# Kernel optimization log

Hardware: AMD Instinct MI355X
Metric: run time of the kernel (lower is better)

Reference implementation:

```python
import jax, jax.numpy as jnp
import numpy as np

N_NODES = 50000
N_EDGES = 800000
NUM_GRAPHS = 250
NODES_PER_GRAPH = 200  # max_len for to_dense_batch
IN_DIM = 128
H1 = 128
H2 = 128
LSTM_H = 128
OUT_DIM = 2
NEG_SLOPE = 0.2  # PyG GATConv default leaky relu slope


def setup_inputs() -> dict:
    key = jax.random.key(0)
    ks = jax.random.split(key, 16)
    x = jax.random.normal(ks[0], (N_NODES, IN_DIM), dtype=jnp.float32)
    edge_index = jax.random.randint(ks[1], (2, N_EDGES), 0, N_NODES, dtype=jnp.int32)
    batch = (jnp.arange(N_NODES, dtype=jnp.int32) // NODES_PER_GRAPH)
    g = lambda k, shp, fan: jax.random.normal(k, shp, dtype=jnp.float32) / np.sqrt(fan)
    return {
        "x": x,
        "edge_index": edge_index,
        "batch": batch,
        "W_gat": g(ks[2], (IN_DIM, H1), IN_DIM),
        "a_src": g(ks[3], (H1,), H1),
        "a_dst": g(ks[4], (H1,), H1),
        "b_gat": jnp.zeros((H1,), jnp.float32),
        "W_gcn": g(ks[5], (H1, H2), H1),
        "b_gcn": jnp.zeros((H2,), jnp.float32),
        "W_ih": g(ks[6], (4 * LSTM_H, H2), H2),
        "W_hh": g(ks[7], (4 * LSTM_H, LSTM_H), LSTM_H),
        "b_ih": jnp.zeros((4 * LSTM_H,), jnp.float32),
        "b_hh": jnp.zeros((4 * LSTM_H,), jnp.float32),
        "W_fc": g(ks[8], (LSTM_H, OUT_DIM), LSTM_H),
        "b_fc": jnp.zeros((OUT_DIM,), jnp.float32),
    }


def _add_self_loops(edge_index, n):
    loop = jnp.arange(n, dtype=edge_index.dtype)
    src = jnp.concatenate([edge_index[0], loop])
    dst = jnp.concatenate([edge_index[1], loop])
    return src, dst


def _gat_conv(x, edge_index, W, a_src, a_dst, b):
    n = x.shape[0]
    h = x @ W                                  # [N, H1]
    src, dst = _add_self_loops(edge_index, n)
    alpha_s = h @ a_src                        # [N]
    alpha_d = h @ a_dst
    e = alpha_s[src] + alpha_d[dst]            # [E+N]
    e = jnp.where(e > 0, e, NEG_SLOPE * e)     # leaky relu
    # softmax over edges sharing the same destination node
    m = jax.ops.segment_max(e, dst, num_segments=n)
    ex = jnp.exp(e - m[dst])
    denom = jax.ops.segment_sum(ex, dst, num_segments=n)
    alpha = ex / denom[dst]
    out = jax.ops.segment_sum(h[src] * alpha[:, None], dst, num_segments=n)
    return out + b


def _gcn_conv(x, edge_index, W, b):
    n = x.shape[0]
    h = x @ W                                  # [N, H2]
    src, dst = _add_self_loops(edge_index, n)
    deg = jax.ops.segment_sum(jnp.ones_like(dst, dtype=h.dtype), dst, num_segments=n)
    dinv = jax.lax.rsqrt(jnp.maximum(deg, 1.0))
    coef = dinv[src] * dinv[dst]               # symmetric normalization
    out = jax.ops.segment_sum(h[src] * coef[:, None], dst, num_segments=n)
    return out + b


def _to_dense_batch(x, batch, num_graphs, max_len):
    n = x.shape[0]
    ones = jnp.ones((n,), jnp.int32)
    counts = jax.ops.segment_sum(ones, batch, num_segments=num_graphs)
    starts = jnp.cumsum(counts) - counts
    pos = jnp.arange(n, dtype=jnp.int32) - starts[batch]
    padded = jnp.zeros((num_graphs, max_len, x.shape[1]), x.dtype)
    padded = padded.at[batch, pos].set(x)
    return padded, counts


def _lstm_last_hidden(padded, lengths, W_ih, W_hh, b_ih, b_hh):
    B, T, D = padded.shape
    H = W_hh.shape[1]
    xs = jnp.swapaxes(padded, 0, 1)            # [T, B, D]

    def step(carry, x_t):
        h, c = carry
        gates = x_t @ W_ih.T + b_ih + h @ W_hh.T + b_hh
        i, f, g, o = jnp.split(gates, 4, axis=-1)
        c = jax.nn.sigmoid(f) * c + jax.nn.sigmoid(i) * jnp.tanh(g)
        h = jax.nn.sigmoid(o) * jnp.tanh(c)
        return (h, c), h

    init = (jnp.zeros((B, H), padded.dtype), jnp.zeros((B, H), padded.dtype))
    _, hs = jax.lax.scan(step, init, xs)       # hs: [T, B, H]
    # packed-sequence semantics: hidden state at each graph's last valid step
    return hs[lengths - 1, jnp.arange(B)]


def reference(x, edge_index, batch, W_gat, a_src, a_dst, b_gat, W_gcn, b_gcn,
              W_ih, W_hh, b_ih, b_hh, W_fc, b_fc):
    h = jax.nn.relu(_gat_conv(x, edge_index, W_gat, a_src, a_dst, b_gat))
    h = jax.nn.relu(_gcn_conv(h, edge_index, W_gcn, b_gcn))
    padded, lengths = _to_dense_batch(h, batch, NUM_GRAPHS, NODES_PER_GRAPH)
    g_rep = _lstm_last_hidden(padded, lengths, W_ih, W_hh, b_ih, b_hh)
    return g_rep @ W_fc + b_fc
```

## Files before the change

### kernel.cpp

```cpp
#include <hip/hip_runtime.h>
#include <cstddef>

#define NN 50000
#define NE 800000
#define NG 250
#define TT 200
#define DD 128
#define GH 512
#define NEG_SLOPE 0.2f
#define NCHUNK 4
#define CLEN 50
#define CAP 128
#define PSTRIDE 136
#define CSTRIDE 132
#define GRIDM ((NG * TT + 63) / 64)

typedef __attribute__((ext_vector_type(8))) short bf16x8;
typedef __attribute__((ext_vector_type(4))) float f32x4;

static __device__ __forceinline__ float fsig(float x) { return 1.0f / (1.0f + __expf(-x)); }
static __device__ __forceinline__ float ftanh(float x) {
    float e = __expf(2.0f * x);
    return 1.0f - 2.0f / (e + 1.0f);
}
static __device__ __forceinline__ unsigned short f2bf(float f) {
    unsigned int u = __float_as_uint(f);
    return (unsigned short)((u + 0x7fffu + ((u >> 16) & 1u)) >> 16);
}
static __device__ __forceinline__ float bf2f(unsigned short b) {
    return __uint_as_float(((unsigned int)b) << 16);
}

static __device__ __forceinline__ void gll16(const void* src, void* ldsdst) {
    __builtin_amdgcn_global_load_lds(
        (const __attribute__((address_space(1))) void*)src,
        (__attribute__((address_space(3))) void*)ldsdst, 16, 0, 0);
}

__global__ void k_init(int* cnt, int* gstart, int n, int ng1) {
    int i = blockIdx.x * 256 + threadIdx.x;
    if (i < n) cnt[i] = 1;
    if (i < ng1) gstart[i] = n;
}

__global__ __launch_bounds__(256) void k_prep(
    const float* __restrict__ Wgat, float* __restrict__ WgatT,
    const float* __restrict__ Wgcn, float* __restrict__ WgcnT,
    const float* __restrict__ Wih, unsigned short* __restrict__ wih_hi,
    unsigned short* __restrict__ wih_lo)
{
    int i = blockIdx.x * 256 + threadIdx.x;
    if (i < 16384) {
        int b = i >> 7, k = i & 127;
        WgatT[b * DD + k] = Wgat[k * DD + b];
    } else if (i < 32768) {
        int j = i - 16384, b = j >> 7, k = j & 127;
        WgcnT[b * DD + k] = Wgcn[k * DD + b];
    }
    float v = Wih[i];
    unsigned short hi = f2bf(v);
    wih_hi[i] = hi;
    wih_lo[i] = f2bf(v - bf2f(hi));
}

__global__ __launch_bounds__(256) void k_gemm(
    const float* __restrict__ A, const float* __restrict__ B, float* __restrict__ C,
    int M, int N, int t0, int clen, int rowsPerGraph,
    const float* __restrict__ bias1, const float* __restrict__ bias2,
    unsigned short* __restrict__ Cbf,
    float* __restrict__ as_out, float* __restrict__ ad_out,
    const float* __restrict__ a_src, const float* __restrict__ a_dst)
{
    __shared__ float4 As[2][1024];
    __shared__ float4 Bs[2][1024];
    const int tid = threadIdx.x;
    const int wv = tid >> 6;
    const int m0 = blockIdx.x * 128, n0 = blockIdx.y * 128;
    const int tr = tid >> 4, tc = tid & 15;

    float acc[8][8];
    #pragma unroll
    for (int i = 0; i < 8; ++i)
        #pragma unroll
        for (int j = 0; j < 8; ++j) acc[i][j] = 0.f;

    auto stageA = [&](int buf, int k0) {
        #pragma unroll
        for (int it = 0; it < 4; ++it) {
            int f4 = it * 256 + tid;
            int r = f4 >> 3;
            int c4s = (f4 & 7) ^ (r & 7);
            int gr = m0 + r;
            float* dst = (float*)&As[buf][it * 256 + wv * 64];
            if (gr < M) {
                int flat = (gr / clen) * rowsPerGraph + t0 + (gr % clen);
                gll16(A + (size_t)flat * DD + k0 + c4s * 4, dst);
            }
        }
    };
    auto stageB = [&](int buf, int k0) {
        #pragma unroll
        for (int it = 0; it < 4; ++it) {
            int f4 = it * 256 + tid;
            int r = f4 >> 3;
            int c4s = (f4 & 7) ^ (r & 7);
            int gn = n0 + r;
            float* dst = (float*)&Bs[buf][it * 256 + wv * 64];
            if (gn < N) gll16(B + (size_t)gn * DD + k0 + c4s * 4, dst);
        }
    };

    stageA(0, 0); stageB(0, 0);
    __syncthreads();
    int buf = 0;
    const int axor = tr & 7;
    const int bxor = tc & 7;
    for (int ks = 0; ks < 4; ++ks) {
        if (ks < 3) { stageA(buf ^ 1, (ks + 1) * 32); stageB(buf ^ 1, (ks + 1) * 32); }
        const float4* Af = &As[buf][0];
        const float4* Bf = &Bs[buf][0];
        #pragma unroll 1
        for (int k4 = 0; k4 < 8; ++k4) {
            float4 a[8], b[8];
            #pragma unroll
            for (int i = 0; i < 8; ++i) a[i] = Af[(tr + i * 16) * 8 + (k4 ^ axor)];
            #pragma unroll
            for (int j = 0; j < 8; ++j) b[j] = Bf[(tc + j * 16) * 8 + (k4 ^ bxor)];
            #pragma unroll
            for (int i = 0; i < 8; ++i)
                #pragma unroll
                for (int j = 0; j < 8; ++j)
                    acc[i][j] += a[i].x * b[j].x + a[i].y * b[j].y + a[i].z * b[j].z + a[i].w * b[j].w;
        }
        __syncthreads();
        buf ^= 1;
    }

    if (as_out) {
        float asv[8], adv[8];
        #pragma unroll
        for (int j = 0; j < 8; ++j) { asv[j] = a_src[tc + 16 * j]; adv[j] = a_dst[tc + 16 * j]; }
        #pragma unroll
        for (int i = 0; i < 8; ++i) {
            float s = 0.f, d = 0.f;
            #pragma unroll
            for (int j = 0; j < 8; ++j) { s += acc[i][j] * asv[j]; d += acc[i][j] * adv[j]; }
            #pragma unroll
            for (int off = 1; off < 16; off <<= 1) { s += __shfl_xor(s, off); d += __shfl_xor(d, off); }
            int gr = m0 + tr + i * 16;
            if (tc == 0 && gr < M) { as_out[gr] = s; ad_out[gr] = d; }
        }
    }

    #pragma unroll
    for (int i = 0; i < 8; ++i) {
        int gr = m0 + tr + i * 16;
        if (gr >= M) continue;
        #pragma unroll
        for (int j = 0; j < 8; ++j) {
            int gn = n0 + tc + j * 16;
            if (gn >= N) continue;
            float v = acc[i][j];
            if (bias1) v += bias1[gn];
            if (bias2) v += bias2[gn];
            if (Cbf) Cbf[(size_t)gr * N + gn] = f2bf(v);
            else     C[(size_t)gr * N + gn] = v;
        }
    }
}

__global__ __launch_bounds__(256) void k_gemm_mx(
    const unsigned short* __restrict__ Ahi, const unsigned short* __restrict__ Alo,
    const unsigned short* __restrict__ Bhi, const unsigned short* __restrict__ Blo,
    float* __restrict__ C, int M,
    const float* __restrict__ bias1, const float* __restrict__ bias2)
{
    __shared__ unsigned short AsH[64 * 128];
    __shared__ unsigned short AsL[64 * 128];
    __shared__ float Cs[64 * CSTRIDE];
    const int tid = threadIdx.x;
    const int wv = tid >> 6;
    const int l = tid & 63;
    const int m0 = blockIdx.x * 64;
    const int wr = (wv >> 1) * 32, wc = (wv & 1) * 64;
    const int lr = l & 15, kg = l >> 4;

    #pragma unroll
    for (int it = 0; it < 4; ++it) {
        int f = it * 256 + tid;
        int r = f >> 4, c8 = f & 15;
        int c8s = c8 ^ (r & 15);
        int gr = m0 + r;
        unsigned short* dstH = &AsH[(it * 256 + wv * 64) * 8];
        unsigned short* dstL = &AsL[(it * 256 + wv * 64) * 8];
        if (gr < M) {
            gll16(Ahi + (size_t)gr * DD + c8s * 8, dstH);
            gll16(Alo + (size_t)gr * DD + c8s * 8, dstL);
        }
    }
    __syncthreads();

    #pragma unroll 1
    for (int cg = 0; cg < 4; ++cg) {
        const int n0 = cg * 128;
        f32x4 acc[2][4];
        #pragma unroll
        for (int rt = 0; rt < 2; ++rt)
            #pragma unroll
            for (int ct = 0; ct < 4; ++ct) acc[rt][ct] = (f32x4){0.f, 0.f, 0.f, 0.f};

        #pragma unroll 1
        for (int ks = 0; ks < 4; ++ks) {
            const int qc = ks * 4 + kg;
            bf16x8 bhi[4], blo[4];
            #pragma unroll
            for (int ct = 0; ct < 4; ++ct) {
                size_t boff = (size_t)(n0 + wc + ct * 16 + lr) * DD + qc * 8;
                bhi[ct] = *(const bf16x8*)(Bhi + boff);
                blo[ct] = *(const bf16x8*)(Blo + boff);
            }
            bf16x8 ahi[2], alo[2];
            #pragma unroll
            for (int rt = 0; rt < 2; ++rt) {
                int row = wr + rt * 16 + lr;
                int slot = row * 16 + (qc ^ (row & 15));
                ahi[rt] = *(const bf16x8*)(&AsH[slot * 8]);
                alo[rt] = *(const bf16x8*)(&AsL[slot * 8]);
            }
            #pragma unroll
            for (int rt = 0; rt < 2; ++rt)
                #pragma unroll
                for (int ct = 0; ct < 4; ++ct) {
                    acc[rt][ct] = __builtin_amdgcn_mfma_f32_16x16x32_bf16(ahi[rt], bhi[ct], acc[rt][ct], 0, 0, 0);
                    acc[rt][ct] = __builtin_amdgcn_mfma_f32_16x16x32_bf16(alo[rt], bhi[ct], acc[rt][ct], 0, 0, 0);
                    acc[rt][ct] = __builtin_amdgcn_mfma_f32_16x16x32_bf16(ahi[rt], blo[ct], acc[rt][ct], 0, 0, 0);
                }
        }

        __syncthreads();
        #pragma unroll
        for (int ct = 0; ct < 4; ++ct) {
            int col = wc + ct * 16 + lr;
            float bsum = bias1[n0 + col] + bias2[n0 + col];
            #pragma unroll
            for (int rt = 0; rt < 2; ++rt) {
                int row = wr + rt * 16 + kg * 4;
                #pragma unroll
                for (int r = 0; r < 4; ++r)
                    Cs[(row + r) * CSTRIDE + col] = acc[rt][ct][r] + bsum;
            }
        }
        __syncthreads();
        #pragma unroll
        for (int it = 0; it < 8; ++it) {
            int f4 = it * 256 + tid;
            int r = f4 >> 5, c4 = f4 & 31;
            int gr = m0 + r;
            if (gr < M)
                *(float4*)(C + (size_t)gr * GH + n0 + c4 * 4) = *(const float4*)(&Cs[r * CSTRIDE + c4 * 4]);
        }
    }
}

__global__ __launch_bounds__(256) void k_gemm_mx128(
    const float* __restrict__ A, const float* __restrict__ Bw,
    unsigned short* __restrict__ Cbf, int M,
    float* __restrict__ as_out, float* __restrict__ ad_out,
    const float* __restrict__ a_src, const float* __restrict__ a_dst)
{
    __shared__ float4 As[4096];
    const int tid = threadIdx.x;
    const int wv = tid >> 6;
    const int l = tid & 63;
    const int lr = l & 15, kg = l >> 4;
    const int m0 = blockIdx.x * 128;
    const int rowbase = wv * 32;

    #pragma unroll
    for (int it = 0; it < 16; ++it) {
        int f4 = it * 256 + tid;
        int r = f4 >> 5, c4 = f4 & 31;
        int c4s = c4 ^ (r & 7);
        int gr = m0 + r;
        float* dst = (float*)&As[it * 256 + wv * 64];
        if (gr < M) gll16(A + (size_t)gr * DD + c4s * 4, dst);
    }
    __syncthreads();

    f32x4 acc[2][8];
    #pragma unroll
    for (int rt = 0; rt < 2; ++rt)
        #pragma unroll
        for (int ct = 0; ct < 8; ++ct) acc[rt][ct] = (f32x4){0.f, 0.f, 0.f, 0.f};

    #pragma unroll 1
    for (int ks = 0; ks < 4; ++ks) {
        bf16x8 bh[8];
        #pragma unroll
        for (int ct = 0; ct < 8; ++ct) {
            const float* brow = Bw + (size_t)(ct * 16 + lr) * DD + ks * 32 + kg * 8;
            float4 f0 = *(const float4*)brow;
            float4 f1 = *(const float4*)(brow + 4);
            float ff[8] = {f0.x, f0.y, f0.z, f0.w, f1.x, f1.y, f1.z, f1.w};
            #pragma unroll
            for (int j = 0; j < 8; ++j) bh[ct][j] = (short)f2bf(ff[j]);
        }
        bf16x8 ahi[2], alo[2];
        #pragma unroll
        for (int rt = 0; rt < 2; ++rt) {
            int row = rowbase + rt * 16 + lr;
            int qb = ks * 8 + kg * 2;
            float4 f0 = As[row * 32 + (qb ^ (row & 7))];
            float4 f1 = As[row * 32 + ((qb + 1) ^ (row & 7))];
            float ff[8] = {f0.x, f0.y, f0.z, f0.w, f1.x, f1.y, f1.z, f1.w};
            #pragma unroll
            for (int j = 0; j < 8; ++j) {
                unsigned short hi = f2bf(ff[j]);
                ahi[rt][j] = (short)hi;
                alo[rt][j] = (short)f2bf(ff[j] - bf2f(hi));
            }
        }
        #pragma unroll
        for (int rt = 0; rt < 2; ++rt)
            #pragma unroll
            for (int ct = 0; ct < 8; ++ct) {
                acc[rt][ct] = __builtin_amdgcn_mfma_f32_16x16x32_bf16(ahi[rt], bh[ct], acc[rt][ct], 0, 0, 0);
                acc[rt][ct] = __builtin_amdgcn_mfma_f32_16x16x32_bf16(alo[rt], bh[ct], acc[rt][ct], 0, 0, 0);
            }
    }
    #pragma unroll 1
    for (int ks = 0; ks < 4; ++ks) {
        bf16x8 bl[8];
        #pragma unroll
        for (int ct = 0; ct < 8; ++ct) {
            const float* brow = Bw + (size_t)(ct * 16 + lr) * DD + ks * 32 + kg * 8;
            float4 f0 = *(const float4*)brow;
            float4 f1 = *(const float4*)(brow + 4);
            float ff[8] = {f0.x, f0.y, f0.z, f0.w, f1.x, f1.y, f1.z, f1.w};
            #pragma unroll
            for (int j = 0; j < 8; ++j)
                bl[ct][j] = (short)f2bf(ff[j] - bf2f(f2bf(ff[j])));
        }
        bf16x8 ahi[2];
        #pragma unroll
        for (int rt = 0; rt < 2; ++rt) {
            int row = rowbase + rt * 16 + lr;
            int qb = ks * 8 + kg * 2;
            float4 f0 = As[row * 32 + (qb ^ (row & 7))];
            float4 f1 = As[row * 32 + ((qb + 1) ^ (row & 7))];
            float ff[8] = {f0.x, f0.y, f0.z, f0.w, f1.x, f1.y, f1.z, f1.w};
            #pragma unroll
            for (int j = 0; j < 8; ++j) ahi[rt][j] = (short)f2bf(ff[j]);
        }
        #pragma unroll
        for (int rt = 0; rt < 2; ++rt)
            #pragma unroll
            for (int ct = 0; ct < 8; ++ct)
                acc[rt][ct] = __builtin_amdgcn_mfma_f32_16x16x32_bf16(ahi[rt], bl[ct], acc[rt][ct], 0, 0, 0);
    }

    #pragma unroll
    for (int rt = 0; rt < 2; ++rt)
        #pragma unroll
        for (int ct = 0; ct < 8; ++ct) {
            int row = m0 + rowbase + rt * 16 + kg * 4;
            int col = ct * 16 + lr;
            #pragma unroll
            for (int r = 0; r < 4; ++r)
                if (row + r < M) Cbf[(size_t)(row + r) * DD + col] = f2bf(acc[rt][ct][r]);
        }
    if (as_out) {
        #pragma unroll
        for (int rt = 0; rt < 2; ++rt)
            #pragma unroll
            for (int r = 0; r < 4; ++r) {
                float s = 0.f, d = 0.f;
                #pragma unroll
                for (int ct = 0; ct < 8; ++ct) {
                    int col = ct * 16 + lr;
                    s += acc[rt][ct][r] * a_src[col];
                    d += acc[rt][ct][r] * a_dst[col];
                }
                #pragma unroll
                for (int off = 1; off < 16; off <<= 1) {
                    s += __shfl_xor(s, off);
                    d += __shfl_xor(d, off);
                }
                int row = m0 + rowbase + rt * 16 + kg * 4 + r;
                if (lr == 0 && row < M) { as_out[row] = s; ad_out[row] = d; }
            }
    }
}

__global__ void k_hist(const int* __restrict__ ei, int* cnt, int E) {
    int e = blockIdx.x * 256 + threadIdx.x;
    if (e < E) atomicAdd(&cnt[ei[E + e]], 1);
}

__global__ __launch_bounds__(256) void k_scan1(const int* __restrict__ cnt, int* __restrict__ fill,
                                               int* __restrict__ bsum, int n) {
    __shared__ int wsum[4];
    int tid = threadIdx.x, lane = tid & 63, wv = tid >> 6;
    int i = blockIdx.x * 256 + tid;
    int v = (i < n) ? cnt[i] : 0;
    int sc = v;
    #pragma unroll
    for (int off = 1; off < 64; off <<= 1) {
        int t = __shfl_up(sc, off);
        if (lane >= off) sc += t;
    }
    if (lane == 63) wsum[wv] = sc;
    __syncthreads();
    int base = 0;
    if (wv > 0) base += wsum[0];
    if (wv > 1) base += wsum[1];
    if (wv > 2) base += wsum[2];
    if (i < n) fill[i] = base + sc - v;
    if (tid == 255) bsum[blockIdx.x] = base + sc;
}
__global__ __launch_bounds__(256) void k_scan2(int* __restrict__ bsum, int nb) {
    __shared__ int wsum[4];
    int tid = threadIdx.x, lane = tid & 63, wv = tid >> 6;
    int v = (tid < nb) ? bsum[tid] : 0;
    int sc = v;
    #pragma unroll
    for (int off = 1; off < 64; off <<= 1) {
        int t = __shfl_up(sc, off);
        if (lane >= off) sc += t;
    }
    if (lane == 63) wsum[wv] = sc;
    __syncthreads();
    int base = 0;
    if (wv > 0) base += wsum[0];
    if (wv > 1) base += wsum[1];
    if (wv > 2) base += wsum[2];
    if (tid < nb) bsum[tid] = base + sc - v;
}
__global__ void k_scan3(const int* __restrict__ bsum, const int* __restrict__ cnt,
                        int* __restrict__ rp, int* __restrict__ fill,
                        float* __restrict__ dinv, const int* __restrict__ batch,
                        int* __restrict__ gstart, int n) {
    int i = blockIdx.x * 256 + threadIdx.x;
    if (i >= n) return;
    int v = fill[i] + bsum[blockIdx.x];
    rp[i] = v;
    fill[i] = v;
    if (i == n - 1) rp[n] = v + cnt[i];
    dinv[i] = rsqrtf(fmaxf((float)cnt[i], 1.0f));
    int b = batch[i];
    if (i == 0 || batch[i - 1] != b) gstart[b] = i;
}

__global__ void k_fill(const int* __restrict__ ei, int* fill, int* esrc, int E, int N) {
    int i = blockIdx.x * 256 + threadIdx.x;
    if (i < E) {
        int s = ei[i], d = ei[E + i];
        int slot = atomicAdd(&fill[d], 1);
        esrc[slot] = s;
    } else if (i < E + N) {
        int v = i - E;
        int slot = atomicAdd(&fill[v], 1);
        esrc[slot] = v;
    }
}

__global__ __launch_bounds__(256) void k_gat(
    const unsigned int* __restrict__ h1b,
    const float* __restrict__ as, const float* __restrict__ ad_,
    const int* __restrict__ rp, const int* __restrict__ esrc,
    const float* __restrict__ bias, float* __restrict__ out, int n)
{
    __shared__ float2 ws_sh[4][CAP];
    int wv = threadIdx.x >> 6;
    int node = blockIdx.x * 4 + wv;
    int lane = threadIdx.x & 63;
    if (node >= n) return;
    int r0 = rp[node], r1 = rp[node + 1];
    int deg = r1 - r0;
    float adv = ad_[node];

    float sum = 0.f;
    for (int base = 0; base < deg; base += 64) {
        int idx = base + lane;
        float ex = 0.f;
        if (idx < deg) {
            int s = esrc[r0 + idx];
            float e = as[s] + adv;
            e = e > 0.f ? e : NEG_SLOPE * e;
            ex = __expf(e);
            if (idx < CAP) ws_sh[wv][idx] = make_float2(ex, __int_as_float(s));
        }
        sum += ex;
    }
    #pragma unroll
    for (int off = 1; off < 64; off <<= 1) sum += __shfl_xor(sum, off);
    float inv = 1.0f / sum;

    int nser = deg < CAP ? deg : CAP;
    int npad = (nser + 7) & ~7;
    for (int p = nser + lane; p < npad; p += 64)
        ws_sh[wv][p] = make_float2(0.f, __int_as_float(0));

    float ax = 0.f, ay = 0.f;
    float wa[8]; unsigned int va[8];
    #pragma unroll
    for (int u = 0; u < 8; ++u) {
        float2 t = ws_sh[wv][u];
        wa[u] = t.x; va[u] = h1b[(size_t)__float_as_int(t.y) * 64 + lane];
    }
    #pragma unroll 1
    for (int idx = 8; idx < npad; idx += 8) {
        float wb[8]; unsigned int vb[8];
        #pragma unroll
        for (int u = 0; u < 8; ++u) {
            float2 t = ws_sh[wv][idx + u];
            wb[u] = t.x; vb[u] = h1b[(size_t)__float_as_int(t.y) * 64 + lane];
        }
        #pragma unroll
        for (int u = 0; u < 8; ++u) {
            ax += wa[u] * __uint_as_float(va[u] << 16);
            ay += wa[u] * __uint_as_float(va[u] & 0xffff0000u);
        }
        #pragma unroll
        for (int u = 0; u < 8; ++u) { wa[u] = wb[u]; va[u] = vb[u]; }
    }
    #pragma unroll
    for (int u = 0; u < 8; ++u) {
        ax += wa[u] * __uint_as_float(va[u] << 16);
        ay += wa[u] * __uint_as_float(va[u] & 0xffff0000u);
    }

    for (int j = r0 + CAP; j < r1; ++j) {
        int s = esrc[j];
        float e = as[s] + adv;
        e = e > 0.f ? e : NEG_SLOPE * e;
        float w = __expf(e);
        unsigned int v = h1b[(size_t)s * 64 + lane];
        ax += w * __uint_as_float(v << 16);
        ay += w * __uint_as_float(v & 0xffff0000u);
    }
    float2 bv = *(const float2*)(bias + 2 * lane);
    float2 o;
    o.x = fmaxf(ax * inv + bv.x, 0.f);
    o.y = fmaxf(ay * inv + bv.y, 0.f);
    *(float2*)(out + (size_t)node * DD + 2 * lane) = o;
}

__global__ __launch_bounds__(256) void k_gcn(
    const unsigned int* __restrict__ h2b, const float* __restrict__ dinv,
    const int* __restrict__ rp, const int* __restrict__ esrc,
    const float* __restrict__ bias, const int* __restrict__ batch,
    const int* __restrict__ gstart, float* __restrict__ padded,
    unsigned short* __restrict__ ph, unsigned short* __restrict__ pl, int n)
{
    __shared__ float2 cs_sh[4][CAP];
    int wv = threadIdx.x >> 6;
    int node = blockIdx.x * 4 + wv;
    int lane = threadIdx.x & 63;
    if (node >= n) return;
    int r0 = rp[node], r1 = rp[node + 1];
    int deg = r1 - r0;
    float dn = dinv[node];

    for (int base = 0; base < deg; base += 64) {
        int idx = base + lane;
        if (idx < deg && idx < CAP) {
            int s = esrc[r0 + idx];
            cs_sh[wv][idx] = make_float2(dinv[s], __int_as_float(s));
        }
    }
    int nser = deg < CAP ? deg : CAP;
    int npad = (nser + 7) & ~7;
    for (int p = nser + lane; p < npad; p += 64)
        cs_sh[wv][p] = make_float2(0.f, __int_as_float(0));
    __syncthreads();

    float ax = 0.f, ay = 0.f;
    float wa[8]; unsigned int va[8];
    #pragma unroll
    for (int u = 0; u < 8; ++u) {
        float2 t = cs_sh[wv][u];
        wa[u] = t.x; va[u] = h2b[(size_t)__float_as_int(t.y) * 64 + lane];
    }
    #pragma unroll 1
    for (int idx = 8; idx < npad; idx += 8) {
        float wb[8]; unsigned int vb[8];
        #pragma unroll
        for (int u = 0; u < 8; ++u) {
            float2 t = cs_sh[wv][idx + u];
            wb[u] = t.x; vb[u] = h2b[(size_t)__float_as_int(t.y) * 64 + lane];
        }
        #pragma unroll
        for (int u = 0; u < 8; ++u) {
            ax += wa[u] * __uint_as_float(va[u] << 16);
            ay += wa[u] * __uint_as_float(va[u] & 0xffff0000u);
        }
        #pragma unroll
        for (int u = 0; u < 8; ++u) { wa[u] = wb[u]; va[u] = vb[u]; }
    }
    #pragma unroll
    for (int u = 0; u < 8; ++u) {
        ax += wa[u] * __uint_as_float(va[u] << 16);
        ay += wa[u] * __uint_as_float(va[u] & 0xffff0000u);
    }

    for (int j = r0 + CAP; j < r1; ++j) {
        int s = esrc[j];
        float c = dinv[s];
        unsigned int v = h2b[(size_t)s * 64 + lane];
        ax += c * __uint_as_float(v << 16);
        ay += c * __uint_as_float(v & 0xffff0000u);
    }
    int g = batch[node];
    if (g < 0 || g >= NG) return;
    int p = node - gstart[g];
    if (p < 0 || p >= TT) return;
    float2 bv = *(const float2*)(bias + 2 * lane);
    float vx = fmaxf(ax * dn + bv.x, 0.f);
    float vy = fmaxf(ay * dn + bv.y, 0.f);
    size_t row = (size_t)g * TT + p;
    if (ph) {
        unsigned short hx = f2bf(vx), hy = f2bf(vy);
        *(ushort2*)(ph + row * DD + 2 * lane) = make_ushort2(hx, hy);
        *(ushort2*)(pl + row * DD + 2 * lane) =
            make_ushort2(f2bf(vx - bf2f(hx)), f2bf(vy - bf2f(hy)));
    } else {
        *(float2*)(padded + row * DD + 2 * lane) = make_float2(vx, vy);
    }
}

__global__ __launch_bounds__(512) void k_lstm(
    const float* __restrict__ xw, const float* __restrict__ Whh,
    const int* __restrict__ gstart,
    float* __restrict__ hstate, float* __restrict__ cstate,
    float* __restrict__ grep, int t0, int clen)
{
    int g = blockIdx.x, tid = threadIdx.x;
    __shared__ __align__(16) float h_sh[DD];
    __shared__ __align__(16) float part[4][4 * PSTRIDE];

    const int seg = tid >> 7;
    const int gq  = tid & 127;
    const int qt  = gq >> 5;
    const int ub  = (gq & 31) * 4;
    const int u   = tid >> 2;
    const int q   = tid & 3;
    const int lane = tid & 63;
    const int qbase = lane & ~3;

    float4 w[4][8];
    #pragma unroll
    for (int g4 = 0; g4 < 4; ++g4)
        #pragma unroll
        for (int i = 0; i < 8; ++i)
            w[g4][i] = *(const float4*)(Whh + (size_t)(4 * gq + g4) * DD + seg * 32 + i * 4);

    float creg = 0.f, hn = 0.f;
    if (t0 == 0) {
        if (tid < DD) h_sh[tid] = 0.f;
    } else {
        creg = cstate[g * DD + u];
        hn = hstate[g * DD + u];
        if (q == 0) h_sh[u] = hn;
    }
    int take = gstart[g + 1] - gstart[g] - 1;
    if (take < 0) take = 0;
    if (take > TT - 1) take = TT - 1;
    __syncthreads();

    const float* xb = xw + (size_t)g * clen * GH + q * DD + u;
    float xv = xb[0];

    for (int t = t0; t < t0 + clen; ++t) {
        int rel = t - t0;
        float xvn = 0.f;
        if (rel + 1 < clen) xvn = xb[(size_t)(rel + 1) * GH];

        float4 hseg[8];
        #pragma unroll
        for (int i = 0; i < 8; ++i) hseg[i] = *(const float4*)(h_sh + seg * 32 + i * 4);
        float p0 = 0.f, p1 = 0.f, p2 = 0.f, p3 = 0.f;
        #pragma unroll
        for (int i = 0; i < 8; ++i) {
            float4 h4 = hseg[i];
            p0 += h4.x * w[0][i].x + h4.y * w[0][i].y + h4.z * w[0][i].z + h4.w * w[0][i].w;
            p1 += h4.x * w[1][i].x + h4.y * w[1][i].y + h4.z * w[1][i].z + h4.w * w[1][i].w;
            p2 += h4.x * w[2][i].x + h4.y * w[2][i].y + h4.z * w[2][i].z + h4.w * w[2][i].w;
            p3 += h4.x * w[3][i].x + h4.y * w[3][i].y + h4.z * w[3][i].z + h4.w * w[3][i].w;
        }
        *(float4*)(&part[seg][qt * PSTRIDE + ub]) = make_float4(p0, p1, p2, p3);
        __syncthreads();

        int pidx = q * PSTRIDE + u;
        float G = xv + part[0][pidx] + part[1][pidx] + part[2][pidx] + part[3][pidx];
        float a = (q == 2) ? 2.f : -1.f;
        float e = __expf(a * G);
        float act = (q == 2) ? (1.f - 2.f / (e + 1.f)) : (1.f / (1.f + e));
        float ai = __shfl(act, qbase + 0);
        float af = __shfl(act, qbase + 1);
        float ag = __shfl(act, qbase + 2);
        float ao = __shfl(act, qbase + 3);
        creg = af * creg + ai * ag;
        hn = ao * ftanh(creg);
        if (q == 0) {
            h_sh[u] = hn;
            if (t == take) grep[g * DD + u] = hn;
        }
        xv = xvn;
        __syncthreads();
    }
    if (q == 0) { hstate[g * DD + u] = hn; cstate[g * DD + u] = creg; }
}

__global__ void k_fc(const float* __restrict__ grep, const float* __restrict__ Wfc,
                     const float* __restrict__ bfc, float* __restrict__ out, int G) {
    int i = blockIdx.x * 256 + threadIdx.x;
    if (i >= G * 2) return;
    int g = i >> 1, o = i & 1;
    float acc = bfc[o];
    for (int d = 0; d < DD; ++d) acc += grep[g * DD + d] * Wfc[d * 2 + o];
    out[i] = acc;
}

extern "C" void kernel_launch(void* const* d_in, const int* in_sizes, int n_in,
                              void* d_out, int out_size, void* d_ws, size_t ws_size,
                              hipStream_t stream) {
    const float* x     = (const float*)d_in[0];
    const int*   ei    = (const int*)d_in[1];
    const int*   batch = (const int*)d_in[2];
    const float* Wgat  = (const float*)d_in[3];
    const float* a_src = (const float*)d_in[4];
    const float* a_dst = (const float*)d_in[5];
    const float* b_gat = (const float*)d_in[6];
    const float* Wgcn  = (const float*)d_in[7];
    const float* b_gcn = (const float*)d_in[8];
    const float* Wih   = (const float*)d_in[9];
    const float* Whh   = (const float*)d_in[10];
    const float* b_ih  = (const float*)d_in[11];
    const float* b_hh  = (const float*)d_in[12];
    const float* Wfc   = (const float*)d_in[13];
    const float* b_fc  = (const float*)d_in[14];
    float* out = (float*)d_out;

    float* ws = (float*)d_ws;
    const size_t F = (size_t)NN * DD;
    unsigned short* h1b = (unsigned short*)ws;
    unsigned short* h2b = (unsigned short*)ws;
    float* xwChunk = ws;
    float* gato   = ws + F;
    float* padded = ws + F;
    unsigned short* padded_hi = (unsigned short*)(ws + F);
    unsigned short* padded_lo = padded_hi + F;
    size_t off = 2 * F;
    float* alpha_s = ws + off; off += 50048;
    float* alpha_d = ws + off; off += 50048;
    float* dinv    = ws + off; off += 50048;
    int*   cnt     = (int*)(ws + off); off += 50048;
    int*   rp      = (int*)(ws + off); off += 50056;
    int*   fill    = (int*)(ws + off); off += 50048;
    int*   esrc    = (int*)(ws + off); off += 850048;
    int*   bsum    = (int*)(ws + off); off += 256;
    int*   gstart  = (int*)(ws + off); off += 256;
    float* grep    = ws + off; off += 32000;
    float* hstate  = ws + off; off += 32000;
    float* cstate  = ws + off; off += 32000;
    float* WgatT   = ws + off; off += 16384;
    float* WgcnT   = ws + off; off += 16384;
    unsigned short* wih_hi = (unsigned short*)(ws + off); off += 32768;
    unsigned short* wih_lo = (unsigned short*)(ws + off); off += 32768;
    const size_t xwBigFloats = (size_t)NG * TT * GH;
    float* xwBig = ws + off;
    const bool big = ws_size >= (off + xwBigFloats) * sizeof(float);

    k_prep<<<256, 256, 0, stream>>>(Wgat, WgatT, Wgcn, WgcnT, Wih, wih_hi, wih_lo);

    if (big) {
        k_gemm_mx128<<<391, 256, 0, stream>>>(x, WgatT, h1b, NN,
                                              alpha_s, alpha_d, a_src, a_dst);
    } else {
        k_gemm<<<dim3(391, 1), 256, 0, stream>>>(x, WgatT, nullptr, NN, DD, 0, TT, TT,
                                                 nullptr, nullptr, h1b,
                                                 alpha_s, alpha_d, a_src, a_dst);
    }

    k_init<<<196, 256, 0, stream>>>(cnt, gstart, NN, NG + 1);
    k_hist<<<3125, 256, 0, stream>>>(ei, cnt, NE);
    k_scan1<<<196, 256, 0, stream>>>(cnt, fill, bsum, NN);
    k_scan2<<<1, 256, 0, stream>>>(bsum, 196);
    k_scan3<<<196, 256, 0, stream>>>(bsum, cnt, rp, fill, dinv, batch, gstart, NN);
    k_fill<<<3321, 256, 0, stream>>>(ei, fill, esrc, NE, NN);

    k_gat<<<12500, 256, 0, stream>>>((const unsigned int*)h1b, alpha_s, alpha_d,
                                     rp, esrc, b_gat, gato, NN);

    if (big) {
        k_gemm_mx128<<<391, 256, 0, stream>>>(gato, WgcnT, h2b, NN,
                                              nullptr, nullptr, nullptr, nullptr);
    } else {
        k_gemm<<<dim3(391, 1), 256, 0, stream>>>(gato, WgcnT, nullptr, NN, DD, 0, TT, TT,
                                                 nullptr, nullptr, h2b,
                                                 nullptr, nullptr, nullptr, nullptr);
    }

    if (big) {
        k_gcn<<<12500, 256, 0, stream>>>((const unsigned int*)h2b, dinv, rp, esrc,
                                         b_gcn, batch, gstart, nullptr,
                                         padded_hi, padded_lo, NN);
    } else {
        k_gcn<<<12500, 256, 0, stream>>>((const unsigned int*)h2b, dinv, rp, esrc,
                                         b_gcn, batch, gstart, padded,
                                         nullptr, nullptr, NN);
    }

    if (big) {
        k_gemm_mx<<<GRIDM, 256, 0, stream>>>(padded_hi, padded_lo, wih_hi, wih_lo,
                                             xwBig, NG * TT, b_ih, b_hh);
        k_lstm<<<NG, 512, 0, stream>>>(xwBig, Whh, gstart, hstate, cstate, grep, 0, TT);
    } else {
        for (int c = 0; c < NCHUNK; ++c) {
            int t0 = c * CLEN;
            k_gemm<<<dim3(98, 4), 256, 0, stream>>>(padded, Wih, xwChunk, NG * CLEN, GH,
                                                    t0, CLEN, TT, b_ih, b_hh,
                                                    nullptr, nullptr, nullptr, nullptr, nullptr);
            k_lstm<<<NG, 512, 0, stream>>>(xwChunk, Whh, gstart, hstate, cstate, grep, t0, CLEN);
        }
    }

    k_fc<<<2, 256, 0, stream>>>(grep, Wfc, b_fc, out, NG);
}
```

Measured before the change: 506.6 us.

## Pre-split GEMM operands into bf16 hi/lo and parallelize LSTM input GEMM columns

Moves the fp32-to-bf16 hi/lo splitting out of the k_gemm_mx128 inner loop. Weights are now split once in k_prep, x in a new k_splitx kernel, and the GAT output directly in k_gat's epilogue, so the GEMM only loads ready bf16 fragments. The GEMM also fuses its three MFMA passes into a single k-loop. k_gemm_mx now spreads its four 128-column groups across gridDim.y instead of looping over them in one block, which raises parallelism but reloads the A tile four times. The cost is an extra elementwise pass over x and more workspace memory.

```diff
diff --git a/kernel.cpp b/kernel.cpp
--- a/kernel.cpp
+++ b/kernel.cpp
@@ -45,22 +45,42 @@
 
 __global__ __launch_bounds__(256) void k_prep(
     const float* __restrict__ Wgat, float* __restrict__ WgatT,
+    unsigned short* __restrict__ wgatT_hi, unsigned short* __restrict__ wgatT_lo,
     const float* __restrict__ Wgcn, float* __restrict__ WgcnT,
+    unsigned short* __restrict__ wgcnT_hi, unsigned short* __restrict__ wgcnT_lo,
     const float* __restrict__ Wih, unsigned short* __restrict__ wih_hi,
     unsigned short* __restrict__ wih_lo)
 {
     int i = blockIdx.x * 256 + threadIdx.x;
     if (i < 16384) {
         int b = i >> 7, k = i & 127;
-        WgatT[b * DD + k] = Wgat[k * DD + b];
+        float v = Wgat[k * DD + b];
+        WgatT[i] = v;
+        unsigned short hi = f2bf(v);
+        wgatT_hi[i] = hi;
+        wgatT_lo[i] = f2bf(v - bf2f(hi));
     } else if (i < 32768) {
         int j = i - 16384, b = j >> 7, k = j & 127;
-        WgcnT[b * DD + k] = Wgcn[k * DD + b];
+        float v = Wgcn[k * DD + b];
+        WgcnT[j] = v;
+        unsigned short hi = f2bf(v);
+        wgcnT_hi[j] = hi;
+        wgcnT_lo[j] = f2bf(v - bf2f(hi));
     }
     float v = Wih[i];
     unsigned short hi = f2bf(v);
     wih_hi[i] = hi;
     wih_lo[i] = f2bf(v - bf2f(hi));
+}
+
+__global__ void k_splitx(const float* __restrict__ x, unsigned short* __restrict__ xh,
+                         unsigned short* __restrict__ xl, int n) {
+    int i = blockIdx.x * 256 + threadIdx.x;
+    if (i >= n) return;
+    float v = x[i];
+    unsigned short hi = f2bf(v);
+    xh[i] = hi;
+    xl[i] = f2bf(v - bf2f(hi));
 }
 
 __global__ __launch_bounds__(256) void k_gemm(
@@ -182,6 +202,7 @@
     const int wv = tid >> 6;
     const int l = tid & 63;
     const int m0 = blockIdx.x * 64;
+    const int n0 = blockIdx.y * 128;
     const int wr = (wv >> 1) * 32, wc = (wv & 1) * 64;
     const int lr = l & 15, kg = l >> 4;
 
@@ -200,75 +221,72 @@
     }
     __syncthreads();
 
+    f32x4 acc[2][4];
+    #pragma unroll
+    for (int rt = 0; rt < 2; ++rt)
+        #pragma unroll
+        for (int ct = 0; ct < 4; ++ct) acc[rt][ct] = (f32x4){0.f, 0.f, 0.f, 0.f};
+
     #pragma unroll 1
-    for (int cg = 0; cg < 4; ++cg) {
-        const int n0 = cg * 128;
-        f32x4 acc[2][4];
+    for (int ks = 0; ks < 4; ++ks) {
+        const int qc = ks * 4 + kg;
+        bf16x8 bhi[4], blo[4];
+        #pragma unroll
+        for (int ct = 0; ct < 4; ++ct) {
+            size_t boff = (size_t)(n0 + wc + ct * 16 + lr) * DD + qc * 8;
+            bhi[ct] = *(const bf16x8*)(Bhi + boff);
+            blo[ct] = *(const bf16x8*)(Blo + boff);
+        }
+        bf16x8 ahi[2], alo[2];
+        #pragma unroll
+        for (int rt = 0; rt < 2; ++rt) {
+            int row = wr + rt * 16 + lr;
+            int slot = row * 16 + (qc ^ (row & 15));
+            ahi[rt] = *(const bf16x8*)(&AsH[slot * 8]);
+            alo[rt] = *(const bf16x8*)(&AsL[slot * 8]);
+        }
         #pragma unroll
         for (int rt = 0; rt < 2; ++rt)
             #pragma unroll
-            for (int ct = 0; ct < 4; ++ct) acc[rt][ct] = (f32x4){0.f, 0.f, 0.f, 0.f};
-
-        #pragma unroll 1
-        for (int ks = 0; ks < 4; ++ks) {
-            const int qc = ks * 4 + kg;
-            bf16x8 bhi[4], blo[4];
-            #pragma unroll
             for (int ct = 0; ct < 4; ++ct) {
-                size_t boff = (size_t)(n0 + wc + ct * 16 + lr) * DD + qc * 8;
-                bhi[ct] = *(const bf16x8*)(Bhi + boff);
-                blo[ct] = *(const bf16x8*)(Blo + boff);
+                acc[rt][ct] = __builtin_amdgcn_mfma_f32_16x16x32_bf16(ahi[rt], bhi[ct], acc[rt][ct], 0, 0, 0);
+                acc[rt][ct] = __builtin_amdgcn_mfma_f32_16x16x32_bf16(alo[rt], bhi[ct], acc[rt][ct], 0, 0, 0);
+                acc[rt][ct] = __builtin_amdgcn_mfma_f32_16x16x32_bf16(ahi[rt], blo[ct], acc[rt][ct], 0, 0, 0);
             }
-            bf16x8 ahi[2], alo[2];
-            #pragma unroll
-            for (int rt = 0; rt < 2; ++rt) {
-                int row = wr + rt * 16 + lr;
-                int slot = row * 16 + (qc ^ (row & 15));
-                ahi[rt] = *(const bf16x8*)(&AsH[slot * 8]);
-                alo[rt] = *(const bf16x8*)(&AsL[slot * 8]);
-            }
-            #pragma unroll
-            for (int rt = 0; rt < 2; ++rt)
-                #pragma unroll
-                for (int ct = 0; ct < 4; ++ct) {
-                    acc[rt][ct] = __builtin_amdgcn_mfma_f32_16x16x32_bf16(ahi[rt], bhi[ct], acc[rt][ct], 0, 0, 0);
-                    acc[rt][ct] = __builtin_amdgcn_mfma_f32_16x16x32_bf16(alo[rt], bhi[ct], acc[rt][ct], 0, 0, 0);
-                    acc[rt][ct] = __builtin_amdgcn_mfma_f32_16x16x32_bf16(ahi[rt], blo[ct], acc[rt][ct], 0, 0, 0);
-                }
-        }
-
-        __syncthreads();
-        #pragma unroll
-        for (int ct = 0; ct < 4; ++ct) {
-            int col = wc + ct * 16 + lr;
-            float bsum = bias1[n0 + col] + bias2[n0 + col];
-            #pragma unroll
-            for (int rt = 0; rt < 2; ++rt) {
-                int row = wr + rt * 16 + kg * 4;
-                #pragma unroll
-                for (int r = 0; r < 4; ++r)
-                    Cs[(row + r) * CSTRIDE + col] = acc[rt][ct][r] + bsum;
-            }
-        }
-        __syncthreads();
-        #pragma unroll
-        for (int it = 0; it < 8; ++it) {
-            int f4 = it * 256 + tid;
-            int r = f4 >> 5, c4 = f4 & 31;
-            int gr = m0 + r;
-            if (gr < M)
-                *(float4*)(C + (size_t)gr * GH + n0 + c4 * 4) = *(const float4*)(&Cs[r * CSTRIDE + c4 * 4]);
-        }
+    }
+
+    #pragma unroll
+    for (int ct = 0; ct < 4; ++ct) {
+        int col = wc + ct * 16 + lr;
+        float bsum = bias1[n0 + col] + bias2[n0 + col];
+        #pragma unroll
+        for (int rt = 0; rt < 2; ++rt) {
+            int row = wr + rt * 16 + kg * 4;
+            #pragma unroll
+            for (int r = 0; r < 4; ++r)
+                Cs[(row + r) * CSTRIDE + col] = acc[rt][ct][r] + bsum;
+        }
+    }
+    __syncthreads();
+    #pragma unroll
+    for (int it = 0; it < 8; ++it) {
+        int f4 = it * 256 + tid;
+        int r = f4 >> 5, c4 = f4 & 31;
+        int gr = m0 + r;
+        if (gr < M)
+            *(float4*)(C + (size_t)gr * GH + n0 + c4 * 4) = *(const float4*)(&Cs[r * CSTRIDE + c4 * 4]);
     }
 }
 
 __global__ __launch_bounds__(256) void k_gemm_mx128(
-    const float* __restrict__ A, const float* __restrict__ Bw,
+    const unsigned short* __restrict__ Ahi, const unsigned short* __restrict__ Alo,
+    const unsigned short* __restrict__ Bhi, const unsigned short* __restrict__ Blo,
     unsigned short* __restrict__ Cbf, int M,
     float* __restrict__ as_out, float* __restrict__ ad_out,
     const float* __restrict__ a_src, const float* __restrict__ a_dst)
 {
-    __shared__ float4 As[4096];
+    __shared__ unsigned short AsH[128 * 128];
+    __shared__ unsigned short AsL[128 * 128];
     const int tid = threadIdx.x;
     const int wv = tid >> 6;
     const int l = tid & 63;
@@ -277,13 +295,17 @@
     const int rowbase = wv * 32;
 
     #pragma unroll
-    for (int it = 0; it < 16; ++it) {
-        int f4 = it * 256 + tid;
-        int r = f4 >> 5, c4 = f4 & 31;
-        int c4s = c4 ^ (r & 7);
+    for (int it = 0; it < 8; ++it) {
+        int f = it * 256 + tid;
+        int r = f >> 4, c8 = f & 15;
+        int c8s = c8 ^ (r & 15);
         int gr = m0 + r;
-        float* dst = (float*)&As[it * 256 + wv * 64];
-        if (gr < M) gll16(A + (size_t)gr * DD + c4s * 4, dst);
+        unsigned short* dstH = &AsH[(it * 256 + wv * 64) * 8];
+        unsigned short* dstL = &AsL[(it * 256 + wv * 64) * 8];
+        if (gr < M) {
+            gll16(Ahi + (size_t)gr * DD + c8s * 8, dstH);
+            gll16(Alo + (size_t)gr * DD + c8s * 8, dstL);
+        }
     }
     __syncthreads();
 
@@ -295,68 +317,30 @@
 
     #pragma unroll 1
     for (int ks = 0; ks < 4; ++ks) {
-        bf16x8 bh[8];
+        const int qc = ks * 4 + kg;
+        bf16x8 bhi[8], blo[8];
         #pragma unroll
         for (int ct = 0; ct < 8; ++ct) {
-            const float* brow = Bw + (size_t)(ct * 16 + lr) * DD + ks * 32 + kg * 8;
-            float4 f0 = *(const float4*)brow;
-            float4 f1 = *(const float4*)(brow + 4);
-            float ff[8] = {f0.x, f0.y, f0.z, f0.w, f1.x, f1.y, f1.z, f1.w};
-            #pragma unroll
-            for (int j = 0; j < 8; ++j) bh[ct][j] = (short)f2bf(ff[j]);
+            size_t boff = (size_t)(ct * 16 + lr) * DD + qc * 8;
+            bhi[ct] = *(const bf16x8*)(Bhi + boff);
+            blo[ct] = *(const bf16x8*)(Blo + boff);
         }
         bf16x8 ahi[2], alo[2];
         #pragma unroll
         for (int rt = 0; rt < 2; ++rt) {
             int row = rowbase + rt * 16 + lr;
-            int qb = ks * 8 + kg * 2;
-            float4 f0 = As[row * 32 + (qb ^ (row & 7))];
-            float4 f1 = As[row * 32 + ((qb + 1) ^ (row & 7))];
-            float ff[8] = {f0.x, f0.y, f0.z, f0.w, f1.x, f1.y, f1.z, f1.w};
-            #pragma unroll
-            for (int j = 0; j < 8; ++j) {
-                unsigned short hi = f2bf(ff[j]);
-                ahi[rt][j] = (short)hi;
-                alo[rt][j] = (short)f2bf(ff[j] - bf2f(hi));
+            int slot = row * 16 + (qc ^ (row & 15));
+            ahi[rt] = *(const bf16x8*)(&AsH[slot * 8]);
+            alo[rt] = *(const bf16x8*)(&AsL[slot * 8]);
+        }
+        #pragma unroll
+        for (int rt = 0; rt < 2; ++rt)
+            #pragma unroll
+            for (int ct = 0; ct < 8; ++ct) {
+                acc[rt][ct] = __builtin_amdgcn_mfma_f32_16x16x32_bf16(ahi[rt], bhi[ct], acc[rt][ct], 0, 0, 0);
+                acc[rt][ct] = __builtin_amdgcn_mfma_f32_16x16x32_bf16(alo[rt], bhi[ct], acc[rt][ct], 0, 0, 0);
+                acc[rt][ct] = __builtin_amdgcn_mfma_f32_16x16x32_bf16(ahi[rt], blo[ct], acc[rt][ct], 0, 0, 0);
             }
-        }
-        #pragma unroll
-        for (int rt = 0; rt < 2; ++rt)
-            #pragma unroll
-            for (int ct = 0; ct < 8; ++ct) {
-                acc[rt][ct] = __builtin_amdgcn_mfma_f32_16x16x32_bf16(ahi[rt], bh[ct], acc[rt][ct], 0, 0, 0);
-                acc[rt][ct] = __builtin_amdgcn_mfma_f32_16x16x32_bf16(alo[rt], bh[ct], acc[rt][ct], 0, 0, 0);
-            }
-    }
-    #pragma unroll 1
-    for (int ks = 0; ks < 4; ++ks) {
-        bf16x8 bl[8];
-        #pragma unroll
-        for (int ct = 0; ct < 8; ++ct) {
-            const float* brow = Bw + (size_t)(ct * 16 + lr) * DD + ks * 32 + kg * 8;
-            float4 f0 = *(const float4*)brow;
-            float4 f1 = *(const float4*)(brow + 4);
-            float ff[8] = {f0.x, f0.y, f0.z, f0.w, f1.x, f1.y, f1.z, f1.w};
-            #pragma unroll
-            for (int j = 0; j < 8; ++j)
-                bl[ct][j] = (short)f2bf(ff[j] - bf2f(f2bf(ff[j])));
-        }
-        bf16x8 ahi[2];
-        #pragma unroll
-        for (int rt = 0; rt < 2; ++rt) {
-            int row = rowbase + rt * 16 + lr;
-            int qb = ks * 8 + kg * 2;
-            float4 f0 = As[row * 32 + (qb ^ (row & 7))];
-            float4 f1 = As[row * 32 + ((qb + 1) ^ (row & 7))];
-            float ff[8] = {f0.x, f0.y, f0.z, f0.w, f1.x, f1.y, f1.z, f1.w};
-            #pragma unroll
-            for (int j = 0; j < 8; ++j) ahi[rt][j] = (short)f2bf(ff[j]);
-        }
-        #pragma unroll
-        for (int rt = 0; rt < 2; ++rt)
-            #pragma unroll
-            for (int ct = 0; ct < 8; ++ct)
-                acc[rt][ct] = __builtin_amdgcn_mfma_f32_16x16x32_bf16(ahi[rt], bl[ct], acc[rt][ct], 0, 0, 0);
     }
 
     #pragma unroll
@@ -468,7 +452,8 @@
     const unsigned int* __restrict__ h1b,
     const float* __restrict__ as, const float* __restrict__ ad_,
     const int* __restrict__ rp, const int* __restrict__ esrc,
-    const float* __restrict__ bias, float* __restrict__ out, int n)
+    const float* __restrict__ bias, float* __restrict__ out,
+    unsigned short* __restrict__ oh, unsigned short* __restrict__ ol, int n)
 {
     __shared__ float2 ws_sh[4][CAP];
     int wv = threadIdx.x >> 6;
@@ -540,10 +525,16 @@
         ay += w * __uint_as_float(v & 0xffff0000u);
     }
     float2 bv = *(const float2*)(bias + 2 * lane);
-    float2 o;
-    o.x = fmaxf(ax * inv + bv.x, 0.f);
-    o.y = fmaxf(ay * inv + bv.y, 0.f);
-    *(float2*)(out + (size_t)node * DD + 2 * lane) = o;
+    float vx = fmaxf(ax * inv + bv.x, 0.f);
+    float vy = fmaxf(ay * inv + bv.y, 0.f);
+    if (oh) {
+        unsigned short hx = f2bf(vx), hy = f2bf(vy);
+        *(ushort2*)(oh + (size_t)node * DD + 2 * lane) = make_ushort2(hx, hy);
+        *(ushort2*)(ol + (size_t)node * DD + 2 * lane) =
+            make_ushort2(f2bf(vx - bf2f(hx)), f2bf(vy - bf2f(hy)));
+    } else {
+        *(float2*)(out + (size_t)node * DD + 2 * lane) = make_float2(vx, vy);
+    }
 }
 
 __global__ __launch_bounds__(256) void k_gcn(
@@ -749,6 +740,8 @@
     float* xwChunk = ws;
     float* gato   = ws + F;
     float* padded = ws + F;
+    unsigned short* gato_hi = (unsigned short*)(ws + F);
+    unsigned short* gato_lo = gato_hi + F;
     unsigned short* padded_hi = (unsigned short*)(ws + F);
     unsigned short* padded_lo = padded_hi + F;
     size_t off = 2 * F;
@@ -768,14 +761,23 @@
     float* WgcnT   = ws + off; off += 16384;
     unsigned short* wih_hi = (unsigned short*)(ws + off); off += 32768;
     unsigned short* wih_lo = (unsigned short*)(ws + off); off += 32768;
+    unsigned short* wgatT_hi = (unsigned short*)(ws + off); off += 8192;
+    unsigned short* wgatT_lo = (unsigned short*)(ws + off); off += 8192;
+    unsigned short* wgcnT_hi = (unsigned short*)(ws + off); off += 8192;
+    unsigned short* wgcnT_lo = (unsigned short*)(ws + off); off += 8192;
+    unsigned short* x_hi = (unsigned short*)(ws + off); off += F / 2;
+    unsigned short* x_lo = (unsigned short*)(ws + off); off += F / 2;
     const size_t xwBigFloats = (size_t)NG * TT * GH;
     float* xwBig = ws + off;
     const bool big = ws_size >= (off + xwBigFloats) * sizeof(float);
 
-    k_prep<<<256, 256, 0, stream>>>(Wgat, WgatT, Wgcn, WgcnT, Wih, wih_hi, wih_lo);
+    k_prep<<<256, 256, 0, stream>>>(Wgat, WgatT, wgatT_hi, wgatT_lo,
+                                    Wgcn, WgcnT, wgcnT_hi, wgcnT_lo,
+                                    Wih, wih_hi, wih_lo);
 
     if (big) {
-        k_gemm_mx128<<<391, 256, 0, stream>>>(x, WgatT, h1b, NN,
+        k_splitx<<<25000, 256, 0, stream>>>(x, x_hi, x_lo, (int)F);
+        k_gemm_mx128<<<391, 256, 0, stream>>>(x_hi, x_lo, wgatT_hi, wgatT_lo, h1b, NN,
                                               alpha_s, alpha_d, a_src, a_dst);
     } else {
         k_gemm<<<dim3(391, 1), 256, 0, stream>>>(x, WgatT, nullptr, NN, DD, 0, TT, TT,
@@ -790,11 +792,16 @@
     k_scan3<<<196, 256, 0, stream>>>(bsum, cnt, rp, fill, dinv, batch, gstart, NN);
     k_fill<<<3321, 256, 0, stream>>>(ei, fill, esrc, NE, NN);
 
-    k_gat<<<12500, 256, 0, stream>>>((const unsigned int*)h1b, alpha_s, alpha_d,
-                                     rp, esrc, b_gat, gato, NN);
-
     if (big) {
-        k_gemm_mx128<<<391, 256, 0, stream>>>(gato, WgcnT, h2b, NN,
+        k_gat<<<12500, 256, 0, stream>>>((const unsigned int*)h1b, alpha_s, alpha_d,
+                                         rp, esrc, b_gat, nullptr, gato_hi, gato_lo, NN);
+    } else {
+        k_gat<<<12500, 256, 0, stream>>>((const unsigned int*)h1b, alpha_s, alpha_d,
+                                         rp, esrc, b_gat, gato, nullptr, nullptr, NN);
+    }
+
+    if (big) {
+        k_gemm_mx128<<<391, 256, 0, stream>>>(gato_hi, gato_lo, wgcnT_hi, wgcnT_lo, h2b, NN,
                                               nullptr, nullptr, nullptr, nullptr);
     } else {
         k_gemm<<<dim3(391, 1), 256, 0, stream>>>(gato, WgcnT, nullptr, NN, DD, 0, TT, TT,
@@ -813,8 +820,9 @@
     }
 
     if (big) {
-        k_gemm_mx<<<GRIDM, 256, 0, stream>>>(padded_hi, padded_lo, wih_hi, wih_lo,
-                                             xwBig, NG * TT, b_ih, b_hh);
+        k_gemm_mx<<<dim3(GRIDM, 4), 256, 0, stream>>>(padded_hi, padded_lo,
+                                                      wih_hi, wih_lo,
+                                                      xwBig, NG * TT, b_ih, b_hh);
         k_lstm<<<NG, 512, 0, stream>>>(xwBig, Whh, gstart, hstate, cstate, grep, 0, TT);
     } else {
         for (int c = 0; c < NCHUNK; ++c) {
```

New measurement: 486.1 us, median of 2. -4.0%, faster.
